# Performance work log

Measured on AMD Instinct MI355X. Metric: run time of the kernel, lower is better.

The kernel has to match this reference:

```python
import jax, jax.numpy as jnp
import numpy as np

TEMPERATURE = 0.07


def setup_inputs() -> dict:
    key = jax.random.key(0)
    k1, k2 = jax.random.split(key)
    B, V, C, H, W = 4, 2, 128, 32, 32
    features = jax.random.normal(k1, (B, V, C, H, W), dtype=jnp.float32)
    # L2-normalize per-pixel feature vectors (channel dim), as contrastive
    # embeddings are in practice; the original exp() is unstabilized.
    features = features / jnp.linalg.norm(features, axis=2, keepdims=True)
    labels = jax.random.randint(k2, (B, V, H, W), 0, 4, dtype=jnp.int32)
    return {"features": features, "labels": labels}


def reference(features, labels):
    B, V, C, H, W = features.shape
    # torch.cat(torch.unbind(features, dim=1), dim=0): views stacked along batch
    cf = jnp.transpose(features, (1, 0, 2, 3, 4)).reshape(B * V, C, H, W)
    # kernels = cf.permute(0,2,3,1).reshape(-1, C, 1, 1); conv2d with 1x1 kernels
    # == pairwise dot products of per-pixel feature vectors.
    X = jnp.transpose(cf, (0, 2, 3, 1)).reshape(-1, C)  # [N, C], N = B*V*H*W
    N = X.shape[0]
    logits = (X @ X.T) / TEMPERATURE  # [N, N]

    lab = jnp.transpose(labels, (1, 0, 2, 3)).reshape(-1)  # [N]
    mask = (lab[:, None] == lab[None, :]).astype(logits.dtype)  # [N, N]
    logits_mask = 1.0 - jnp.eye(N, dtype=logits.dtype)  # zero the diagonal
    mask = mask * logits_mask

    exp_logits = jnp.exp(logits) * logits_mask
    log_prob = logits - jnp.log(jnp.sum(exp_logits, axis=1, keepdims=True))
    mean_log_prob_pos = jnp.sum(mask * log_prob, axis=1) / jnp.sum(mask, axis=1)
    loss = -mean_log_prob_pos  # [N]

    non_bg = (lab != 0).astype(logits.dtype)
    return jnp.sum(loss * non_bg) / jnp.sum(non_bg)
```

## Files before the change

### kernel.cpp

```cpp
#include <hip/hip_runtime.h>
#include <hip/hip_bf16.h>
#include <stdint.h>

typedef short bf16x8 __attribute__((ext_vector_type(8)));
typedef float f32x16 __attribute__((ext_vector_type(16)));

#define NROWS 8192
#define CDIM  128
#define TEMP  0.07f
#define C1F   20.6099291555566248f

#define OFF_S    0
#define OFF_G    32768
#define OFF_HIST (32768 + 2048)
#define OFF_SUM  (32768 + 2048 + 16)
#define OFF_TKT  (32768 + 2048 + 16 + 4)
#define ZBYTES   (32768 + 2048 + 16 + 4 + 4)
#define ZWORDS   (ZBYTES / 4)

__device__ __forceinline__ float bf2f(unsigned short u) {
  union { unsigned int i; float f; } x; x.i = ((unsigned int)u) << 16; return x.f;
}
__device__ __forceinline__ unsigned short f2bf(float f) {
  union { float f; unsigned int i; } x; x.f = f;
  unsigned int r = x.i + 0x7fffu + ((x.i >> 16) & 1u);
  return (unsigned short)(r >> 16);
}
__device__ __forceinline__ float fexp2(float x) {
#if __has_builtin(__builtin_amdgcn_exp2f)
  return __builtin_amdgcn_exp2f(x);
#else
  return exp2f(x);
#endif
}

__global__ __launch_bounds__(256) void k_pack(const float* __restrict__ F,
                                              unsigned short* __restrict__ Xb,
                                              float* __restrict__ zbase) {
  const int tid = threadIdx.x;
  {
    int idx = blockIdx.x * 256 + tid;
    if (idx < ZWORDS) zbase[idx] = 0.0f;
  }
  __shared__ float lds[128 * 33];
  const int g   = blockIdx.x >> 5;
  const int hw0 = (blockIdx.x & 31) << 5;
#pragma unroll
  for (int p = 0; p < 16; ++p) {
    int c  = p * 8 + (tid >> 5);
    int hw = hw0 + (tid & 31);
    lds[c * 33 + (tid & 31)] = F[(g * 128 + c) * 1024 + hw];
  }
  __syncthreads();
#pragma unroll
  for (int p = 0; p < 16; ++p) {
    int hwl = p * 2 + (tid >> 7);
    int c   = tid & 127;
    int row = g * 1024 + hw0 + hwl;
    Xb[row * 128 + c] = f2bf(lds[c * 33 + hwl]);
  }
}

__global__ __launch_bounds__(256, 4) void k_main(const unsigned short* __restrict__ Xb,
                                                 const int* __restrict__ labels,
                                                 float* __restrict__ S,
                                                 float* __restrict__ G,
                                                 int* __restrict__ hist) {
  __shared__ int4 ldsB[2][2][16 * 33];
  const int bid = blockIdx.x;
  const int tid = threadIdx.x;
  const int lane = tid & 63;

  if (bid < 128) {
    const int rchunk = bid >> 3;
    const int cbase  = (bid & 7) * 16;
    const int cl     = tid & 15;
    const int rg     = tid >> 4;
    float a0 = 0.f, a1 = 0.f, a2 = 0.f, a3 = 0.f;
    const int nend = rchunk * 512 + 512;
    for (int n = rchunk * 512 + rg; n < nend; n += 16) {
      int   lab = labels[n];
      float v   = bf2f(Xb[n * 128 + cbase + cl]);
      a0 += (lab == 0) ? v : 0.f;
      a1 += (lab == 1) ? v : 0.f;
      a2 += (lab == 2) ? v : 0.f;
      a3 += (lab == 3) ? v : 0.f;
    }
    a0 += __shfl_xor(a0, 16, 64); a0 += __shfl_xor(a0, 32, 64);
    a1 += __shfl_xor(a1, 16, 64); a1 += __shfl_xor(a1, 32, 64);
    a2 += __shfl_xor(a2, 16, 64); a2 += __shfl_xor(a2, 32, 64);
    a3 += __shfl_xor(a3, 16, 64); a3 += __shfl_xor(a3, 32, 64);
    if (lane < 16) {
      int c = cbase + lane;
      atomicAdd(&G[0 * 128 + c], a0);
      atomicAdd(&G[1 * 128 + c], a1);
      atomicAdd(&G[2 * 128 + c], a2);
      atomicAdd(&G[3 * 128 + c], a3);
    }
    if (bid == 0) {
      int h0 = 0, h1 = 0, h2 = 0, h3 = 0;
      for (int n = tid; n < NROWS; n += 256) {
        int lab = labels[n];
        h0 += (lab == 0); h1 += (lab == 1); h2 += (lab == 2); h3 += (lab == 3);
      }
      for (int mm = 1; mm < 64; mm <<= 1) {
        h0 += __shfl_xor(h0, mm, 64); h1 += __shfl_xor(h1, mm, 64);
        h2 += __shfl_xor(h2, mm, 64); h3 += __shfl_xor(h3, mm, 64);
      }
      if (lane == 0) {
        atomicAdd(&hist[0], h0); atomicAdd(&hist[1], h1);
        atomicAdd(&hist[2], h2); atomicAdd(&hist[3], h3);
      }
    }
    return;
  }

  const int b        = bid - 128;
  const int wave     = tid >> 6;
  const int rowBlock = b >> 4;
  const int split    = b & 15;
  const int r0       = rowBlock * 128 + wave * 32;
  const int col0     = split * 512;
  const int m        = lane & 31;
  const int half     = lane >> 5;

  bf16x8 afrag[8];
#pragma unroll
  for (int s = 0; s < 8; ++s)
    afrag[s] = *(const bf16x8*)(Xb + (r0 + m) * CDIM + (half + 2 * s) * 8);

  float accS[16];
#pragma unroll
  for (int r = 0; r < 16; ++r) accS[r] = 0.f;

  const int n_l = tid >> 3;
  const int bq  = tid & 7;
  const unsigned short* src = Xb + (col0 + n_l) * CDIM + bq * 16;
  int4 v0 = *(const int4*)src;
  int4 v1 = *(const int4*)(src + 8);
  int4 v2 = *(const int4*)(src + 32 * CDIM);
  int4 v3 = *(const int4*)(src + 32 * CDIM + 8);
  ldsB[0][0][(2 * bq) * 33 + n_l]     = v0;
  ldsB[0][0][(2 * bq + 1) * 33 + n_l] = v1;
  ldsB[0][1][(2 * bq) * 33 + n_l]     = v2;
  ldsB[0][1][(2 * bq + 1) * 33 + n_l] = v3;
  src += 64 * CDIM;
  v0 = *(const int4*)src;
  v1 = *(const int4*)(src + 8);
  v2 = *(const int4*)(src + 32 * CDIM);
  v3 = *(const int4*)(src + 32 * CDIM + 8);

  for (int t = 0; t < 8; ++t) {
    __syncthreads();
    if (t < 7) {
      const int nb = (t + 1) & 1;
      ldsB[nb][0][(2 * bq) * 33 + n_l]     = v0;
      ldsB[nb][0][(2 * bq + 1) * 33 + n_l] = v1;
      ldsB[nb][1][(2 * bq) * 33 + n_l]     = v2;
      ldsB[nb][1][(2 * bq + 1) * 33 + n_l] = v3;
    }
    if (t < 6) {
      src += 64 * CDIM;
      v0 = *(const int4*)src;
      v1 = *(const int4*)(src + 8);
      v2 = *(const int4*)(src + 32 * CDIM);
      v3 = *(const int4*)(src + 32 * CDIM + 8);
    }
    const int cur = t & 1;
#pragma unroll
    for (int u = 0; u < 2; ++u) {
      f32x16 acc;
#pragma unroll
      for (int r = 0; r < 16; ++r) acc[r] = 0.f;
#pragma unroll
      for (int s = 0; s < 8; ++s) {
        bf16x8 bfrag = *(const bf16x8*)&ldsB[cur][u][(half + 2 * s) * 33 + m];
        acc = __builtin_amdgcn_mfma_f32_32x32x16_bf16(afrag[s], bfrag, acc, 0, 0, 0);
      }
      const int colbase = col0 + t * 64 + u * 32;
      if (r0 == colbase) {
        const int colg = colbase + m;
#pragma unroll
        for (int r = 0; r < 16; ++r) {
          int   row = r0 + (r & 3) + 8 * (r >> 2) + 4 * half;
          float arg = (row == colg) ? -1e30f : acc[r] * C1F;
          accS[r] += fexp2(arg);
        }
      } else {
#pragma unroll
        for (int r = 0; r < 16; ++r) accS[r] += fexp2(acc[r] * C1F);
      }
    }
  }

#pragma unroll
  for (int r = 0; r < 16; ++r) {
    float v = accS[r];
    v += __shfl_xor(v, 1, 64);
    v += __shfl_xor(v, 2, 64);
    v += __shfl_xor(v, 4, 64);
    v += __shfl_xor(v, 8, 64);
    v += __shfl_xor(v, 16, 64);
    accS[r] = v;
  }
  if (m == 0) {
#pragma unroll
    for (int r = 0; r < 16; ++r) {
      int row = r0 + (r & 3) + 8 * (r >> 2) + 4 * half;
      atomicAdd(&S[row], accS[r]);
    }
  }
}

__global__ __launch_bounds__(256) void k_loss(const unsigned short* __restrict__ Xb,
                                              const int* __restrict__ labels,
                                              const float* __restrict__ S,
                                              const float* __restrict__ G,
                                              const int* __restrict__ hist,
                                              float* __restrict__ sumLoss,
                                              int* __restrict__ ticket,
                                              float* __restrict__ out) {
  const int i   = blockIdx.x * 256 + threadIdx.x;
  const int lab = labels[i];
  const float* g = G + lab * 128;
  const unsigned short* x = Xb + i * CDIM;
  float dot = 0.f, nrm = 0.f;
#pragma unroll
  for (int cc = 0; cc < 16; ++cc) {
    int4 q = *(const int4*)(x + cc * 8);
    const unsigned int* qs = (const unsigned int*)&q;
#pragma unroll
    for (int j = 0; j < 4; ++j) {
      unsigned int u = qs[j];
      float lo = __uint_as_float(u << 16);
      float hi = __uint_as_float(u & 0xffff0000u);
      int   ci = cc * 8 + j * 2;
      dot += lo * g[ci] + hi * g[ci + 1];
      nrm += lo * lo + hi * hi;
    }
  }
  float Si   = S[i];
  float cnt  = (float)(hist[lab] - 1);
  float loss = logf(Si) - (dot - nrm) / (TEMP * cnt);
  float contrib = (lab != 0) ? loss : 0.f;
  for (int mm = 1; mm < 64; mm <<= 1) contrib += __shfl_xor(contrib, mm, 64);
  __shared__ float ws4[4];
  if ((threadIdx.x & 63) == 0) ws4[threadIdx.x >> 6] = contrib;
  __syncthreads();
  if (threadIdx.x == 0) {
    atomicAdd(sumLoss, ws4[0] + ws4[1] + ws4[2] + ws4[3]);
    __threadfence();
    int t = atomicAdd(ticket, 1);
    if (t == 31) {
      float total = atomicAdd(sumLoss, 0.0f);
      out[0] = total / (float)(NROWS - hist[0]);
    }
  }
}

extern "C" void kernel_launch(void* const* d_in, const int* in_sizes, int n_in,
                              void* d_out, int out_size, void* d_ws, size_t ws_size,
                              hipStream_t stream) {
  const float* F      = (const float*)d_in[0];
  const int*   labels = (const int*)d_in[1];
  char* ws = (char*)d_ws;

  unsigned short* Xb      = (unsigned short*)ws;
  const size_t    offS    = (size_t)NROWS * CDIM * 2;
  float*          S       = (float*)(ws + offS + OFF_S);
  float*          G       = (float*)(ws + offS + OFF_G);
  int*            hist    = (int*)(ws + offS + OFF_HIST);
  float*          sumLoss = (float*)(ws + offS + OFF_SUM);
  int*            ticket  = (int*)(ws + offS + OFF_TKT);

  hipLaunchKernelGGL(k_pack, dim3(256), dim3(256), 0, stream, F, Xb, S);
  hipLaunchKernelGGL(k_main, dim3(1152), dim3(256), 0, stream, Xb, labels, S, G, hist);
  hipLaunchKernelGGL(k_loss, dim3(32), dim3(256), 0, stream, Xb, labels, S, G, hist,
                     sumLoss, ticket, (float*)d_out);
}
```

Baseline: 99.76 us.

## Fuse pack, similarity and loss kernels into one flag-synchronized launch

Merges the bf16 pack, the exp-sum GEMM and the loss reduction into a single 1024-block kernel. Per-block MAGIC flags and ticket counters replace the kernel boundaries. Per-split partial sums are written to workspace instead of using float atomics, and the last 32 blocks to finish compute the loss. The class sums are now read directly from the fp32 input, so they no longer wait on the pack. This removes two launch gaps and the atomic contention, but it depends on all blocks being co-resident for the spin-waits. The flags are never cleared between calls, so on repeat runs stale flags can let blocks read data before the current call has rewritten it.

```diff
diff --git a/kernel.cpp b/kernel.cpp
--- a/kernel.cpp
+++ b/kernel.cpp
@@ -9,14 +9,16 @@
 #define CDIM  128
 #define TEMP  0.07f
 #define C1F   20.6099291555566248f
-
-#define OFF_S    0
-#define OFF_G    32768
-#define OFF_HIST (32768 + 2048)
-#define OFF_SUM  (32768 + 2048 + 16)
-#define OFF_TKT  (32768 + 2048 + 16 + 4)
-#define ZBYTES   (32768 + 2048 + 16 + 4 + 4)
-#define ZWORDS   (ZBYTES / 4)
+#define MAGIC 0x13579BDF
+
+#define OFF_SPART 2097152
+#define OFF_GPART 2621440
+#define OFF_HPART 2654208
+#define OFF_SLP   2655232
+#define OFF_PFLAG 2657280
+#define OFF_GFLAG 2658368
+#define OFF_TKT   2658880
+#define OFF_TKT2  2658884
 
 __device__ __forceinline__ float bf2f(unsigned short u) {
   union { unsigned int i; float f; } x; x.i = ((unsigned int)u) << 16; return x.f;
@@ -33,96 +35,140 @@
   return exp2f(x);
 #endif
 }
-
-__global__ __launch_bounds__(256) void k_pack(const float* __restrict__ F,
-                                              unsigned short* __restrict__ Xb,
-                                              float* __restrict__ zbase) {
-  const int tid = threadIdx.x;
+__device__ __forceinline__ int aload(int* p) {
+  return __hip_atomic_load(p, __ATOMIC_RELAXED, __HIP_MEMORY_SCOPE_AGENT);
+}
+__device__ __forceinline__ void astore(int* p, int v) {
+  __hip_atomic_store(p, v, __ATOMIC_RELAXED, __HIP_MEMORY_SCOPE_AGENT);
+}
+
+__global__ __launch_bounds__(256, 4) void k_fused(const float* __restrict__ F,
+                                                  const int* __restrict__ labels,
+                                                  char* __restrict__ ws,
+                                                  float* __restrict__ out) {
+  unsigned short* Xb    = (unsigned short*)ws;
+  float*          Spart = (float*)(ws + OFF_SPART);
+  float*          Gpart = (float*)(ws + OFF_GPART);
+  int*            Hpart = (int*)(ws + OFF_HPART);
+  float*          SLP   = (float*)(ws + OFF_SLP);
+  int*            pflag = (int*)(ws + OFF_PFLAG);
+  int*            gflag = (int*)(ws + OFF_GFLAG);
+  int*            tkt   = (int*)(ws + OFF_TKT);
+  int*            tkt2  = (int*)(ws + OFF_TKT2);
+
+  __shared__ int4 smem4[2112];
+  char* smem = (char*)smem4;
+
+  const int tid  = threadIdx.x;
+  const int bid  = blockIdx.x;
+  const int lane = tid & 63;
+  const int wave = tid >> 6;
+
+  if (bid < 256) {
+    if (bid == 0 && tid == 0) {
+      astore(tkt, 0);
+      astore(tkt2, 0);
+      __hip_atomic_store(&pflag[256], MAGIC, __ATOMIC_RELEASE,
+                         __HIP_MEMORY_SCOPE_AGENT);
+    }
+    {
+      float* lds = (float*)smem;
+      const int g = bid >> 5, hw0 = (bid & 31) << 5;
+#pragma unroll
+      for (int p = 0; p < 16; ++p) {
+        int c  = p * 8 + (tid >> 5);
+        int hw = hw0 + (tid & 31);
+        lds[c * 33 + (tid & 31)] = F[(g * 128 + c) * 1024 + hw];
+      }
+      __syncthreads();
+#pragma unroll
+      for (int p = 0; p < 16; ++p) {
+        int hwl = p * 2 + (tid >> 7);
+        int c   = tid & 127;
+        int row = g * 1024 + hw0 + hwl;
+        Xb[row * 128 + c] = f2bf(lds[c * 33 + hwl]);
+      }
+      __syncthreads();
+      if (tid == 0) {
+        __builtin_amdgcn_fence(__ATOMIC_RELEASE, "agent");
+        astore(&pflag[bid], MAGIC);
+      }
+    }
+    if (bid < 128) {
+      const int rchunk = bid >> 3;
+      const int cbase  = (bid & 7) * 16;
+      const int cl     = tid & 15;
+      const int rg     = tid >> 4;
+      float a0 = 0.f, a1 = 0.f, a2 = 0.f, a3 = 0.f;
+      int   h0 = 0, h1 = 0, h2 = 0, h3 = 0;
+      const bool doHist = ((bid & 7) == 0) && (cl == 0);
+      for (int j = rg; j < 512; j += 16) {
+        int   n   = rchunk * 512 + j;
+        int   lab = labels[n];
+        float v   = bf2f(f2bf(F[((n >> 10) * 128 + cbase + cl) * 1024 + (n & 1023)]));
+        a0 += (lab == 0) ? v : 0.f;
+        a1 += (lab == 1) ? v : 0.f;
+        a2 += (lab == 2) ? v : 0.f;
+        a3 += (lab == 3) ? v : 0.f;
+        if (doHist) { h0 += (lab == 0); h1 += (lab == 1); h2 += (lab == 2); h3 += (lab == 3); }
+      }
+      a0 += __shfl_xor(a0, 16, 64); a0 += __shfl_xor(a0, 32, 64);
+      a1 += __shfl_xor(a1, 16, 64); a1 += __shfl_xor(a1, 32, 64);
+      a2 += __shfl_xor(a2, 16, 64); a2 += __shfl_xor(a2, 32, 64);
+      a3 += __shfl_xor(a3, 16, 64); a3 += __shfl_xor(a3, 32, 64);
+      float* lds_g = (float*)smem;
+      int*   lds_h = (int*)(smem + 1024);
+      if (lane < 16) {
+        lds_g[wave * 64 + 0 * 16 + lane] = a0;
+        lds_g[wave * 64 + 1 * 16 + lane] = a1;
+        lds_g[wave * 64 + 2 * 16 + lane] = a2;
+        lds_g[wave * 64 + 3 * 16 + lane] = a3;
+      }
+      if (doHist) {
+        lds_h[rg * 4 + 0] = h0; lds_h[rg * 4 + 1] = h1;
+        lds_h[rg * 4 + 2] = h2; lds_h[rg * 4 + 3] = h3;
+      }
+      __syncthreads();
+      if (tid < 64) {
+        int l = tid >> 4, c = tid & 15;
+        float s = 0.f;
+#pragma unroll
+        for (int w = 0; w < 4; ++w) s += lds_g[w * 64 + l * 16 + c];
+        Gpart[bid * 64 + l * 16 + c] = s;
+      }
+      if (((bid & 7) == 0) && tid < 4) {
+        int hs = 0;
+#pragma unroll
+        for (int r = 0; r < 16; ++r) hs += lds_h[r * 4 + tid];
+        Hpart[(bid >> 3) * 16 + tid] = hs;
+      }
+      __syncthreads();
+      if (tid == 0) {
+        __builtin_amdgcn_fence(__ATOMIC_RELEASE, "agent");
+        astore(&gflag[bid], MAGIC);
+      }
+    }
+  }
+
+  const int rb   = bid >> 4;
+  const int sp   = bid & 15;
+  const int r0   = rb * 128 + wave * 32;
+  const int col0 = sp * 512;
+  const int m    = lane & 31;
+  const int half = lane >> 5;
+
   {
-    int idx = blockIdx.x * 256 + tid;
-    if (idx < ZWORDS) zbase[idx] = 0.0f;
-  }
-  __shared__ float lds[128 * 33];
-  const int g   = blockIdx.x >> 5;
-  const int hw0 = (blockIdx.x & 31) << 5;
-#pragma unroll
-  for (int p = 0; p < 16; ++p) {
-    int c  = p * 8 + (tid >> 5);
-    int hw = hw0 + (tid & 31);
-    lds[c * 33 + (tid & 31)] = F[(g * 128 + c) * 1024 + hw];
-  }
-  __syncthreads();
-#pragma unroll
-  for (int p = 0; p < 16; ++p) {
-    int hwl = p * 2 + (tid >> 7);
-    int c   = tid & 127;
-    int row = g * 1024 + hw0 + hwl;
-    Xb[row * 128 + c] = f2bf(lds[c * 33 + hwl]);
-  }
-}
-
-__global__ __launch_bounds__(256, 4) void k_main(const unsigned short* __restrict__ Xb,
-                                                 const int* __restrict__ labels,
-                                                 float* __restrict__ S,
-                                                 float* __restrict__ G,
-                                                 int* __restrict__ hist) {
-  __shared__ int4 ldsB[2][2][16 * 33];
-  const int bid = blockIdx.x;
-  const int tid = threadIdx.x;
-  const int lane = tid & 63;
-
-  if (bid < 128) {
-    const int rchunk = bid >> 3;
-    const int cbase  = (bid & 7) * 16;
-    const int cl     = tid & 15;
-    const int rg     = tid >> 4;
-    float a0 = 0.f, a1 = 0.f, a2 = 0.f, a3 = 0.f;
-    const int nend = rchunk * 512 + 512;
-    for (int n = rchunk * 512 + rg; n < nend; n += 16) {
-      int   lab = labels[n];
-      float v   = bf2f(Xb[n * 128 + cbase + cl]);
-      a0 += (lab == 0) ? v : 0.f;
-      a1 += (lab == 1) ? v : 0.f;
-      a2 += (lab == 2) ? v : 0.f;
-      a3 += (lab == 3) ? v : 0.f;
-    }
-    a0 += __shfl_xor(a0, 16, 64); a0 += __shfl_xor(a0, 32, 64);
-    a1 += __shfl_xor(a1, 16, 64); a1 += __shfl_xor(a1, 32, 64);
-    a2 += __shfl_xor(a2, 16, 64); a2 += __shfl_xor(a2, 32, 64);
-    a3 += __shfl_xor(a3, 16, 64); a3 += __shfl_xor(a3, 32, 64);
-    if (lane < 16) {
-      int c = cbase + lane;
-      atomicAdd(&G[0 * 128 + c], a0);
-      atomicAdd(&G[1 * 128 + c], a1);
-      atomicAdd(&G[2 * 128 + c], a2);
-      atomicAdd(&G[3 * 128 + c], a3);
-    }
-    if (bid == 0) {
-      int h0 = 0, h1 = 0, h2 = 0, h3 = 0;
-      for (int n = tid; n < NROWS; n += 256) {
-        int lab = labels[n];
-        h0 += (lab == 0); h1 += (lab == 1); h2 += (lab == 2); h3 += (lab == 3);
-      }
-      for (int mm = 1; mm < 64; mm <<= 1) {
-        h0 += __shfl_xor(h0, mm, 64); h1 += __shfl_xor(h1, mm, 64);
-        h2 += __shfl_xor(h2, mm, 64); h3 += __shfl_xor(h3, mm, 64);
-      }
-      if (lane == 0) {
-        atomicAdd(&hist[0], h0); atomicAdd(&hist[1], h1);
-        atomicAdd(&hist[2], h2); atomicAdd(&hist[3], h3);
-      }
-    }
-    return;
-  }
-
-  const int b        = bid - 128;
-  const int wave     = tid >> 6;
-  const int rowBlock = b >> 4;
-  const int split    = b & 15;
-  const int r0       = rowBlock * 128 + wave * 32;
-  const int col0     = split * 512;
-  const int m        = lane & 31;
-  const int half     = lane >> 5;
+    int fidx = 256;
+    if (tid < 4) fidx = rb * 4 + tid;
+    else if (tid < 20) fidx = sp * 16 + (tid - 4);
+    int ok;
+    do {
+      ok = 1;
+      if (tid < 21) ok = (aload(&pflag[fidx]) == MAGIC);
+      if (!ok) __builtin_amdgcn_s_sleep(2);
+    } while (!__syncthreads_and(ok));
+    __builtin_amdgcn_fence(__ATOMIC_ACQUIRE, "workgroup");
+  }
 
   bf16x8 afrag[8];
 #pragma unroll
@@ -133,6 +179,7 @@
 #pragma unroll
   for (int r = 0; r < 16; ++r) accS[r] = 0.f;
 
+#define LB(buf, u, idx) smem4[((buf) * 2 + (u)) * 528 + (idx)]
   const int n_l = tid >> 3;
   const int bq  = tid & 7;
   const unsigned short* src = Xb + (col0 + n_l) * CDIM + bq * 16;
@@ -140,10 +187,10 @@
   int4 v1 = *(const int4*)(src + 8);
   int4 v2 = *(const int4*)(src + 32 * CDIM);
   int4 v3 = *(const int4*)(src + 32 * CDIM + 8);
-  ldsB[0][0][(2 * bq) * 33 + n_l]     = v0;
-  ldsB[0][0][(2 * bq + 1) * 33 + n_l] = v1;
-  ldsB[0][1][(2 * bq) * 33 + n_l]     = v2;
-  ldsB[0][1][(2 * bq + 1) * 33 + n_l] = v3;
+  LB(0, 0, (2 * bq) * 33 + n_l)     = v0;
+  LB(0, 0, (2 * bq + 1) * 33 + n_l) = v1;
+  LB(0, 1, (2 * bq) * 33 + n_l)     = v2;
+  LB(0, 1, (2 * bq + 1) * 33 + n_l) = v3;
   src += 64 * CDIM;
   v0 = *(const int4*)src;
   v1 = *(const int4*)(src + 8);
@@ -154,10 +201,10 @@
     __syncthreads();
     if (t < 7) {
       const int nb = (t + 1) & 1;
-      ldsB[nb][0][(2 * bq) * 33 + n_l]     = v0;
-      ldsB[nb][0][(2 * bq + 1) * 33 + n_l] = v1;
-      ldsB[nb][1][(2 * bq) * 33 + n_l]     = v2;
-      ldsB[nb][1][(2 * bq + 1) * 33 + n_l] = v3;
+      LB(nb, 0, (2 * bq) * 33 + n_l)     = v0;
+      LB(nb, 0, (2 * bq + 1) * 33 + n_l) = v1;
+      LB(nb, 1, (2 * bq) * 33 + n_l)     = v2;
+      LB(nb, 1, (2 * bq + 1) * 33 + n_l) = v3;
     }
     if (t < 6) {
       src += 64 * CDIM;
@@ -174,7 +221,7 @@
       for (int r = 0; r < 16; ++r) acc[r] = 0.f;
 #pragma unroll
       for (int s = 0; s < 8; ++s) {
-        bf16x8 bfrag = *(const bf16x8*)&ldsB[cur][u][(half + 2 * s) * 33 + m];
+        bf16x8 bfrag = *(const bf16x8*)&LB(cur, u, (half + 2 * s) * 33 + m);
         acc = __builtin_amdgcn_mfma_f32_32x32x16_bf16(afrag[s], bfrag, acc, 0, 0, 0);
       }
       const int colbase = col0 + t * 64 + u * 32;
@@ -207,22 +254,59 @@
 #pragma unroll
     for (int r = 0; r < 16; ++r) {
       int row = r0 + (r & 3) + 8 * (r >> 2) + 4 * half;
-      atomicAdd(&S[row], accS[r]);
-    }
-  }
-}
-
-__global__ __launch_bounds__(256) void k_loss(const unsigned short* __restrict__ Xb,
-                                              const int* __restrict__ labels,
-                                              const float* __restrict__ S,
-                                              const float* __restrict__ G,
-                                              const int* __restrict__ hist,
-                                              float* __restrict__ sumLoss,
-                                              int* __restrict__ ticket,
-                                              float* __restrict__ out) {
-  const int i   = blockIdx.x * 256 + threadIdx.x;
+      Spart[sp * 8192 + row] = accS[r];
+    }
+  }
+
+  __syncthreads();
+  if (tid == 0) {
+    __builtin_amdgcn_fence(__ATOMIC_RELEASE, "agent");
+    int tt = __hip_atomic_fetch_add(tkt, 1, __ATOMIC_RELAXED,
+                                    __HIP_MEMORY_SCOPE_AGENT);
+    ((int*)smem)[0] = tt;
+  }
+  __syncthreads();
+  const int t = ((int*)smem)[0];
+  if (t < 1024 - 32) return;
+
+  const int chunk = t - (1024 - 32);
+  {
+    int ok;
+    do {
+      ok = 1;
+      if (tid < 128)      ok = (aload(&gflag[tid]) == MAGIC);
+      else if (tid < 136) ok = (aload(&pflag[chunk * 8 + tid - 128]) == MAGIC);
+      else if (tid == 136) ok = (aload(tkt) == 1024);
+      if (!ok) __builtin_amdgcn_s_sleep(2);
+    } while (!__syncthreads_and(ok));
+    __builtin_amdgcn_fence(__ATOMIC_ACQUIRE, "workgroup");
+  }
+  float* G_lds = (float*)smem;
+  int*   h_lds = (int*)(smem + 2048);
+  float* red   = (float*)(smem + 2064);
+  int*   comm2 = (int*)(smem + 2080);
+#pragma unroll
+  for (int e = tid; e < 512; e += 256) {
+    int l = e >> 7, c = e & 127;
+    float s = 0.f;
+#pragma unroll
+    for (int r = 0; r < 16; ++r)
+      s += Gpart[(r * 8 + (c >> 4)) * 64 + l * 16 + (c & 15)];
+    G_lds[e] = s;
+  }
+  if (tid < 4) {
+    int hs = 0;
+#pragma unroll
+    for (int r = 0; r < 16; ++r) hs += Hpart[r * 16 + tid];
+    h_lds[tid] = hs;
+  }
+  __syncthreads();
+  const int i   = chunk * 256 + tid;
   const int lab = labels[i];
-  const float* g = G + lab * 128;
+  float Si = 0.f;
+#pragma unroll
+  for (int sp2 = 0; sp2 < 16; ++sp2) Si += Spart[sp2 * 8192 + i];
+  const float* gl = G_lds + lab * 128;
   const unsigned short* x = Xb + i * CDIM;
   float dot = 0.f, nrm = 0.f;
 #pragma unroll
@@ -235,26 +319,34 @@
       float lo = __uint_as_float(u << 16);
       float hi = __uint_as_float(u & 0xffff0000u);
       int   ci = cc * 8 + j * 2;
-      dot += lo * g[ci] + hi * g[ci + 1];
+      dot += lo * gl[ci] + hi * gl[ci + 1];
       nrm += lo * lo + hi * hi;
     }
   }
-  float Si   = S[i];
-  float cnt  = (float)(hist[lab] - 1);
+  float cnt  = (float)(h_lds[lab] - 1);
   float loss = logf(Si) - (dot - nrm) / (TEMP * cnt);
   float contrib = (lab != 0) ? loss : 0.f;
   for (int mm = 1; mm < 64; mm <<= 1) contrib += __shfl_xor(contrib, mm, 64);
-  __shared__ float ws4[4];
-  if ((threadIdx.x & 63) == 0) ws4[threadIdx.x >> 6] = contrib;
-  __syncthreads();
-  if (threadIdx.x == 0) {
-    atomicAdd(sumLoss, ws4[0] + ws4[1] + ws4[2] + ws4[3]);
-    __threadfence();
-    int t = atomicAdd(ticket, 1);
-    if (t == 31) {
-      float total = atomicAdd(sumLoss, 0.0f);
-      out[0] = total / (float)(NROWS - hist[0]);
-    }
+  if (lane == 0) red[wave] = contrib;
+  __syncthreads();
+  if (tid == 0) {
+    float bsum = red[0] + red[1] + red[2] + red[3];
+    __hip_atomic_store(&SLP[chunk * 16], bsum, __ATOMIC_RELAXED,
+                       __HIP_MEMORY_SCOPE_AGENT);
+    int t2 = __hip_atomic_fetch_add(tkt2, 1, __ATOMIC_ACQ_REL,
+                                    __HIP_MEMORY_SCOPE_AGENT);
+    comm2[0] = (t2 == 31) ? 1 : 0;
+  }
+  __syncthreads();
+  if (comm2[0]) {
+    float v = 0.f;
+    if (tid < 32)
+      v = __hip_atomic_load(&SLP[tid * 16], __ATOMIC_RELAXED,
+                            __HIP_MEMORY_SCOPE_AGENT);
+    if (tid < 64) {
+      for (int mm = 1; mm < 32; mm <<= 1) v += __shfl_xor(v, mm, 64);
+    }
+    if (tid == 0) out[0] = v / (float)(NROWS - h_lds[0]);
   }
 }
 
@@ -263,18 +355,6 @@
                               hipStream_t stream) {
   const float* F      = (const float*)d_in[0];
   const int*   labels = (const int*)d_in[1];
-  char* ws = (char*)d_ws;
-
-  unsigned short* Xb      = (unsigned short*)ws;
-  const size_t    offS    = (size_t)NROWS * CDIM * 2;
-  float*          S       = (float*)(ws + offS + OFF_S);
-  float*          G       = (float*)(ws + offS + OFF_G);
-  int*            hist    = (int*)(ws + offS + OFF_HIST);
-  float*          sumLoss = (float*)(ws + offS + OFF_SUM);
-  int*            ticket  = (int*)(ws + offS + OFF_TKT);
-
-  hipLaunchKernelGGL(k_pack, dim3(256), dim3(256), 0, stream, F, Xb, S);
-  hipLaunchKernelGGL(k_main, dim3(1152), dim3(256), 0, stream, Xb, labels, S, G, hist);
-  hipLaunchKernelGGL(k_loss, dim3(32), dim3(256), 0, stream, Xb, labels, S, G, hist,
-                     sumLoss, ticket, (float*)d_out);
-}
+  hipLaunchKernelGGL(k_fused, dim3(1024), dim3(256), 0, stream,
+                     F, labels, (char*)d_ws, (float*)d_out);
+}
```

Result: slower. 125.1 us (+25.4%).
